# Optimization experiments

Hardware: AMD Instinct MI355X
Metric: run time of the kernel (lower is better)

The kernel has to match this reference:

```python
import math
import jax, jax.numpy as jnp
import numpy as np

H = 12
D_MODEL = 768
D_K = D_MODEL // H
B, S = 2, 2048


def setup_inputs() -> dict:
    key = jax.random.key(0)
    ks = jax.random.split(key, 12)
    sc = 0.02
    inp = {
        "query": jax.random.normal(ks[0], (B, S, D_MODEL), jnp.float32),
        "key": jax.random.normal(ks[1], (B, S, D_MODEL), jnp.float32),
        "value": jax.random.normal(ks[2], (B, S, D_MODEL), jnp.float32),
        # causal mask [B, S, S]: 1 where attendable
        "mask": jnp.broadcast_to(jnp.tril(jnp.ones((S, S), jnp.int32)), (B, S, S)),
        "Wq": sc * jax.random.normal(ks[3], (D_MODEL, D_MODEL), jnp.float32),
        "bq": jnp.zeros((D_MODEL,), jnp.float32),
        "Wk": sc * jax.random.normal(ks[4], (D_MODEL, D_MODEL), jnp.float32),
        "bk": jnp.zeros((D_MODEL,), jnp.float32),
        "Wv": sc * jax.random.normal(ks[5], (D_MODEL, D_MODEL), jnp.float32),
        "bv": jnp.zeros((D_MODEL,), jnp.float32),
        "Wo": sc * jax.random.normal(ks[6], (D_MODEL, D_MODEL), jnp.float32),
        "bo": jnp.zeros((D_MODEL,), jnp.float32),
    }
    return inp


def reference(query, key, value, mask, Wq, bq, Wk, bk, Wv, bv, Wo, bo):
    b, s, _ = query.shape
    # linear projections (torch Linear: x @ W.T + b), split into heads
    def proj(x, W, bias):
        return (x @ W.T + bias).reshape(b, s, H, D_K).transpose(0, 2, 1, 3)  # [B,H,S,Dk]

    q = proj(query, Wq, bq)
    k = proj(key, Wk, bk)
    v = proj(value, Wv, bv)

    scores = jnp.einsum("bhqd,bhkd->bhqk", q, k) / math.sqrt(D_K)  # [B,H,S,S]
    # exponential time-decay bias over key positions 1..S, shape [1,1,1,S]
    time = jnp.exp(-jnp.arange(1, s + 1, dtype=scores.dtype))[None, None, None, :]
    scores = jnp.where(mask[:, None, :, :] == 0, jnp.asarray(-1e9, scores.dtype), scores)
    p_attn = jax.nn.softmax(scores - time, axis=-1)
    x = jnp.einsum("bhqk,bhkd->bhqd", p_attn, v)  # [B,H,S,Dk]
    x = x.transpose(0, 2, 1, 3).reshape(b, s, H * D_K)
    return x @ Wo.T + bo
```

## Files before the change

kernel.cpp:

```cpp
#include <hip/hip_runtime.h>
#include <hip/hip_bf16.h>
#include <math.h>

typedef __bf16 bf16;
typedef __attribute__((ext_vector_type(8))) __bf16 bf16x8;
typedef __attribute__((ext_vector_type(4))) __bf16 bf16x4;
typedef __attribute__((ext_vector_type(4))) float floatx4;

#define NH 12
#define DK 64
#define DM 768
#define NB 2
#define SEQ 2048
#define MTOT (NB * SEQ)
#define WELEM (DM * DM)
#define XELEM (MTOT * DM)

static __device__ __forceinline__ bf16x8 load8(const bf16* p) {
    return *(const bf16x8*)p;
}
static __device__ __forceinline__ float4 ld4(const float* p) {
    return *(const float4*)p;
}
static __device__ __forceinline__ bf16x8 cvt8(const float4 a, const float4 b) {
    bf16x8 r;
    r[0] = (bf16)a.x; r[1] = (bf16)a.y; r[2] = (bf16)a.z; r[3] = (bf16)a.w;
    r[4] = (bf16)b.x; r[5] = (bf16)b.y; r[6] = (bf16)b.z; r[7] = (bf16)b.w;
    return r;
}
static __device__ __forceinline__ void async16(const bf16* g, bf16* l) {
    __builtin_amdgcn_global_load_lds((const __attribute__((address_space(1))) void*)g,
                                     (__attribute__((address_space(3))) void*)l,
                                     16, 0, 0);
}

__global__ __launch_bounds__(256) void cvt_kernel(
    const float* __restrict__ wq, const float* __restrict__ wk,
    const float* __restrict__ wv, const float* __restrict__ wo,
    const float* __restrict__ xq, const float* __restrict__ xk, const float* __restrict__ xv,
    bf16* __restrict__ Wb, bf16* __restrict__ Wob,
    bf16* __restrict__ Xqb, bf16* __restrict__ Xkb, bf16* __restrict__ Xvb) {
    const int g = blockIdx.x * 256 + threadIdx.x;
    const int PW = WELEM / 8;
    const int PX = XELEM / 8;
    if (g < 4 * PW) {
        const int wi = g / PW;
        const int rem = g - wi * PW;
        const int n = rem / 96;
        const int t = rem - n * 96;
        const int s = t >> 3;
        const int j = t & 7;
        const float* src = (wi == 0) ? wq : (wi == 1) ? wk : (wi == 2) ? wv : wo;
        bf16* dst = (wi < 3) ? (Wb + (size_t)wi * WELEM) : Wob;
        const float* p = src + (size_t)n * DM + s * 64 + j * 8;
        *(bf16x8*)(dst + (size_t)n * DM + s * 64 + ((j ^ (n & 7)) * 8)) = cvt8(ld4(p), ld4(p + 4));
    } else {
        const int gx = g - 4 * PW;
        const int xi = gx / PX;
        const int rem = gx - xi * PX;
        const int m = rem / 96;
        const int t = rem - m * 96;
        const int s = t >> 3;
        const int j = t & 7;
        const float* src = (xi == 0) ? xq : (xi == 1) ? xk : xv;
        bf16* dst = (xi == 0) ? Xqb : (xi == 1) ? Xkb : Xvb;
        const float* p = src + (size_t)m * DM + s * 64 + j * 8;
        *(bf16x8*)(dst + (size_t)m * DM + s * 64 + ((j ^ (m & 7)) * 8)) = cvt8(ld4(p), ld4(p + 4));
    }
}

__global__ __launch_bounds__(256, 3) void qkv_kernel(
    const bf16* __restrict__ Xqb, const bf16* __restrict__ Xkb, const bf16* __restrict__ Xvb,
    const bf16* __restrict__ Wb,
    const float* __restrict__ bq, const float* __restrict__ bk, const float* __restrict__ bv,
    bf16* __restrict__ Oq, bf16* __restrict__ Ok, bf16* __restrict__ Ov) {
    __shared__ __align__(16) bf16 SM[2 * 64 * 64 + 2 * 128 * 64];
    bf16* As0 = SM;
    bf16* Bs0 = SM + 8192;

    const int tid = threadIdx.x;
    const int id = blockIdx.x;
    const int xcd = id & 7;
    const int sl = id >> 3;
    const int z = sl / 48;
    const int r = sl % 48;
    const int m0 = (xcd * 8 + r / 6) * 64;
    const int n0 = (r % 6) * 128;

    const bf16* X = (z == 0) ? Xqb : (z == 1) ? Xkb : Xvb;
    const bf16* W = Wb + (size_t)z * WELEM;
    const float* bias = (z == 0) ? bq : (z == 1) ? bk : bv;
    bf16* out = (z == 0) ? Oq : (z == 1) ? Ok : Ov;

    const int wv = tid >> 6;
    const int wm = wv >> 1, wn = wv & 1;
    const int lane = tid & 63;
    const int ln = lane & 15;
    const int kq = lane >> 4;
    const int drow = lane >> 3;
    const int dcol = (lane & 7) * 8;

    floatx4 acc[2][4];
#pragma unroll
    for (int i = 0; i < 2; i++)
#pragma unroll
        for (int j = 0; j < 4; j++) acc[i][j] = (floatx4){0.f, 0.f, 0.f, 0.f};

#pragma unroll
    for (int it = 0; it < 2; it++)
        async16(X + (size_t)(m0 + wv * 16 + it * 8 + drow) * DM + dcol,
                As0 + (wv * 16 + it * 8) * 64);
#pragma unroll
    for (int it = 0; it < 4; it++)
        async16(W + (size_t)(n0 + wv * 32 + it * 8 + drow) * DM + dcol,
                Bs0 + (wv * 32 + it * 8) * 64);

    for (int k = 0; k < 12; k++) {
        __syncthreads();
        const bf16* Ap = As0 + (k & 1) * 4096;
        const bf16* Bp = Bs0 + (k & 1) * 8192;
        if (k < 11) {
            const int kc = (k + 1) * 64;
            bf16* An = As0 + ((k + 1) & 1) * 4096;
            bf16* Bn = Bs0 + ((k + 1) & 1) * 8192;
#pragma unroll
            for (int it = 0; it < 2; it++)
                async16(X + (size_t)(m0 + wv * 16 + it * 8 + drow) * DM + kc + dcol,
                        An + (wv * 16 + it * 8) * 64);
#pragma unroll
            for (int it = 0; it < 4; it++)
                async16(W + (size_t)(n0 + wv * 32 + it * 8 + drow) * DM + kc + dcol,
                        Bn + (wv * 32 + it * 8) * 64);
        }
#pragma unroll
        for (int ks = 0; ks < 2; ks++) {
            const int jb = (ks * 4 + kq) ^ (ln & 7);
            bf16x8 af[2], bfm[4];
#pragma unroll
            for (int mt = 0; mt < 2; mt++)
                af[mt] = *(const bf16x8*)&Ap[(wm * 32 + mt * 16 + ln) * 64 + jb * 8];
#pragma unroll
            for (int nt = 0; nt < 4; nt++)
                bfm[nt] = *(const bf16x8*)&Bp[(wn * 64 + nt * 16 + ln) * 64 + jb * 8];
#pragma unroll
            for (int mt = 0; mt < 2; mt++)
#pragma unroll
                for (int nt = 0; nt < 4; nt++)
                    acc[mt][nt] = __builtin_amdgcn_mfma_f32_16x16x32_bf16(af[mt], bfm[nt], acc[mt][nt], 0, 0, 0);
        }
    }

    float bv4[4];
#pragma unroll
    for (int nt = 0; nt < 4; nt++) bv4[nt] = bias[n0 + wn * 64 + nt * 16 + ln];

    if (z < 2) {
        __syncthreads();
        bf16 (*E)[136] = (bf16(*)[136])SM;
#pragma unroll
        for (int mt = 0; mt < 2; mt++)
#pragma unroll
            for (int nt = 0; nt < 4; nt++)
#pragma unroll
                for (int r2 = 0; r2 < 4; r2++)
                    E[wm * 32 + mt * 16 + kq * 4 + r2][wn * 64 + nt * 16 + ln] =
                        (bf16)(acc[mt][nt][r2] + bv4[nt]);
        __syncthreads();
        const int row = tid >> 2;
        const int cb = (tid & 3) * 32;
        const int m = m0 + row;
        const int b = m >> 11;
        const int s = m & (SEQ - 1);
        const int h = (n0 + cb) >> 6;
        const int d = (n0 + cb) & 63;
        bf16* op = &out[((size_t)(b * NH + h) * SEQ + s) * DK + d];
#pragma unroll
        for (int q2 = 0; q2 < 4; q2++)
            *(bf16x8*)(op + q2 * 8) = *(bf16x8*)&E[row][cb + q2 * 8];
    } else {
        __syncthreads();
        bf16 (*E)[72] = (bf16(*)[72])SM;
#pragma unroll
        for (int nt = 0; nt < 4; nt++)
#pragma unroll
            for (int mt = 0; mt < 2; mt++) {
                bf16x4 v;
#pragma unroll
                for (int r2 = 0; r2 < 4; r2++) v[r2] = (bf16)(acc[mt][nt][r2] + bv4[nt]);
                *(bf16x4*)&E[wn * 64 + nt * 16 + ln][wm * 32 + mt * 16 + kq * 4] = v;
            }
        __syncthreads();
        const int row = tid >> 1;
        const int sc = (tid & 1) * 32;
        const int b = m0 >> 11;
        const int s0 = m0 & (SEQ - 1);
        const int h = (n0 >> 6) + (row >> 6);
        const int d = row & 63;
        bf16* op = &out[(size_t)(b * NH + h) * DK * SEQ + (size_t)d * SEQ + s0 + sc];
#pragma unroll
        for (int q2 = 0; q2 < 4; q2++)
            *(bf16x8*)(op + q2 * 8) = *(bf16x8*)&E[row][sc + q2 * 8];
    }
}

__global__ __launch_bounds__(256) void attn_kernel(const bf16* __restrict__ Q,
                                                   const bf16* __restrict__ K,
                                                   const bf16* __restrict__ Vt,
                                                   bf16* __restrict__ Xout) {
    __shared__ bf16 Ks[128][72];
    __shared__ bf16 Vs[64][136];
    __shared__ bf16 Ps[4][16][136];

    const int tid = threadIdx.x;
    const int wv = tid >> 6;
    const int lane = tid & 63;
    const int ln = lane & 15;
    const int kq = lane >> 4;
    const int krow = tid >> 1;
    const int kcol = (tid & 1) * 32;
    const int vrow = tid >> 2;
    const int vcol = (tid & 3) * 32;

    const int bidx = blockIdx.x;
    const int rk = (bidx < 256 || bidx >= 512) ? bidx : 767 - bidx;
    const int x = 31 - (rk / 24);
    const int bh = rk % 24;

    const int q0 = x * 64;
    const int qbase = q0 + wv * 16;
    const int nch = (x >> 1) + 1;

    const bf16* Qb = Q + (size_t)bh * SEQ * DK;
    const bf16* Kb = K + (size_t)bh * SEQ * DK;
    const bf16* Vb = Vt + (size_t)bh * SEQ * DK;

    const bf16x8 qa0 = load8(&Qb[(size_t)(qbase + ln) * DK + kq * 8]);
    const bf16x8 qa1 = load8(&Qb[(size_t)(qbase + ln) * DK + 32 + kq * 8]);

    bf16x8 kx[4], vx[4];
#pragma unroll
    for (int q = 0; q < 4; q++) {
        kx[q] = load8(&Kb[(size_t)krow * DK + kcol + q * 8]);
        vx[q] = load8(&Vb[(size_t)vrow * SEQ + vcol + q * 8]);
    }

    float lsum[4] = {0.f, 0.f, 0.f, 0.f};
    floatx4 Oacc[4];
#pragma unroll
    for (int nt = 0; nt < 4; nt++) Oacc[nt] = (floatx4){0.f, 0.f, 0.f, 0.f};

    int qg[4];
#pragma unroll
    for (int r = 0; r < 4; r++) qg[r] = qbase + kq * 4 + r;

    for (int c = 0; c < nch; c++) {
        const int k0 = c * 128;
        __syncthreads();
#pragma unroll
        for (int q = 0; q < 4; q++) {
            *(bf16x8*)&Ks[krow][kcol + q * 8] = kx[q];
            *(bf16x8*)&Vs[vrow][vcol + q * 8] = vx[q];
        }
        __syncthreads();
        if (c + 1 < nch) {
            const int kn = k0 + 128;
#pragma unroll
            for (int q = 0; q < 4; q++) {
                kx[q] = load8(&Kb[(size_t)(kn + krow) * DK + kcol + q * 8]);
                vx[q] = load8(&Vb[(size_t)vrow * SEQ + kn + vcol + q * 8]);
            }
        }

        floatx4 sc[8];
#pragma unroll
        for (int ks = 0; ks < 8; ks++) {
            const bf16x8 b0 = *(bf16x8*)&Ks[ks * 16 + ln][kq * 8];
            const bf16x8 b1 = *(bf16x8*)&Ks[ks * 16 + ln][32 + kq * 8];
            floatx4 t = (floatx4){0.f, 0.f, 0.f, 0.f};
            t = __builtin_amdgcn_mfma_f32_16x16x32_bf16(qa0, b0, t, 0, 0, 0);
            t = __builtin_amdgcn_mfma_f32_16x16x32_bf16(qa1, b1, t, 0, 0, 0);
            sc[ks] = t;
        }

        const bool last = (c == nch - 1);
#pragma unroll
        for (int ks = 0; ks < 8; ks++) {
            const int kg = k0 + ks * 16 + ln;
            const float tb = __expf(-(float)(kg + 1));
#pragma unroll
            for (int r = 0; r < 4; r++) {
                const float sv = sc[ks][r] * 0.125f - tb;
                float pf = __expf(sv);
                if (last && kg > qg[r]) pf = 0.f;
                const bf16 pb = (bf16)pf;
                Ps[wv][kq * 4 + r][ks * 16 + ln] = pb;
                lsum[r] += (float)pb;
            }
        }

        bf16x8 pa[4];
#pragma unroll
        for (int seg = 0; seg < 4; seg++) pa[seg] = *(bf16x8*)&Ps[wv][ln][seg * 32 + kq * 8];
#pragma unroll
        for (int nt = 0; nt < 4; nt++) {
#pragma unroll
            for (int seg = 0; seg < 4; seg++) {
                const bf16x8 vb = *(bf16x8*)&Vs[nt * 16 + ln][seg * 32 + kq * 8];
                Oacc[nt] = __builtin_amdgcn_mfma_f32_16x16x32_bf16(pa[seg], vb, Oacc[nt], 0, 0, 0);
            }
        }
    }

#pragma unroll
    for (int off = 1; off < 16; off <<= 1) {
#pragma unroll
        for (int r = 0; r < 4; r++) lsum[r] += __shfl_xor(lsum[r], off, 64);
    }
    float rl[4];
#pragma unroll
    for (int r = 0; r < 4; r++) rl[r] = 1.f / lsum[r];

    __syncthreads();
    bf16 (*E)[72] = (bf16(*)[72])Ks;
    const int erow = tid >> 2;
    const int ecb = (tid & 3) * 16;
#pragma unroll
    for (int nt = 0; nt < 4; nt++) {
#pragma unroll
        for (int r = 0; r < 4; r++)
            E[wv * 16 + kq * 4 + r][nt * 16 + ln] = (bf16)(Oacc[nt][r] * rl[r]);
    }
    __syncthreads();
    const int b = bh / NH;
    const int h = bh - b * NH;
    const int q = q0 + erow;
    const int j0 = (tid & 3) * 2;
    const int key = erow & 7;
    bf16* rowp = &Xout[((size_t)(b * SEQ + q)) * DM + h * DK];
    *(bf16x8*)(rowp + ((j0 ^ key) * 8)) = *(bf16x8*)&E[erow][ecb];
    *(bf16x8*)(rowp + (((j0 + 1) ^ key) * 8)) = *(bf16x8*)&E[erow][ecb + 8];
}

__global__ __launch_bounds__(256, 3) void outproj_kernel(const bf16* __restrict__ X,
                                                         const bf16* __restrict__ W,
                                                         const float* __restrict__ bias,
                                                         float* __restrict__ out) {
    __shared__ __align__(16) bf16 SM[2 * 64 * 64 + 2 * 128 * 64];
    bf16* As0 = SM;
    bf16* Bs0 = SM + 8192;

    const int tid = threadIdx.x;
    const int id = blockIdx.x;
    const int xcd = id & 7;
    const int sl = id >> 3;
    const int m0 = (xcd * 8 + sl / 6) * 64;
    const int n0 = (sl % 6) * 128;

    const int wv = tid >> 6;
    const int wm = wv >> 1, wn = wv & 1;
    const int lane = tid & 63;
    const int ln = lane & 15;
    const int kq = lane >> 4;
    const int drow = lane >> 3;
    const int dcol = (lane & 7) * 8;

    floatx4 acc[2][4];
#pragma unroll
    for (int i = 0; i < 2; i++)
#pragma unroll
        for (int j = 0; j < 4; j++) acc[i][j] = (floatx4){0.f, 0.f, 0.f, 0.f};

#pragma unroll
    for (int it = 0; it < 2; it++)
        async16(X + (size_t)(m0 + wv * 16 + it * 8 + drow) * DM + dcol,
                As0 + (wv * 16 + it * 8) * 64);
#pragma unroll
    for (int it = 0; it < 4; it++)
        async16(W + (size_t)(n0 + wv * 32 + it * 8 + drow) * DM + dcol,
                Bs0 + (wv * 32 + it * 8) * 64);

    for (int k = 0; k < 12; k++) {
        __syncthreads();
        const bf16* Ap = As0 + (k & 1) * 4096;
        const bf16* Bp = Bs0 + (k & 1) * 8192;
        if (k < 11) {
            const int kc = (k + 1) * 64;
            bf16* An = As0 + ((k + 1) & 1) * 4096;
            bf16* Bn = Bs0 + ((k + 1) & 1) * 8192;
#pragma unroll
            for (int it = 0; it < 2; it++)
                async16(X + (size_t)(m0 + wv * 16 + it * 8 + drow) * DM + kc + dcol,
                        An + (wv * 16 + it * 8) * 64);
#pragma unroll
            for (int it = 0; it < 4; it++)
                async16(W + (size_t)(n0 + wv * 32 + it * 8 + drow) * DM + kc + dcol,
                        Bn + (wv * 32 + it * 8) * 64);
        }
#pragma unroll
        for (int ks = 0; ks < 2; ks++) {
            const int jb = (ks * 4 + kq) ^ (ln & 7);
            bf16x8 af[2], bfm[4];
#pragma unroll
            for (int mt = 0; mt < 2; mt++)
                af[mt] = *(const bf16x8*)&Ap[(wm * 32 + mt * 16 + ln) * 64 + jb * 8];
#pragma unroll
            for (int nt = 0; nt < 4; nt++)
                bfm[nt] = *(const bf16x8*)&Bp[(wn * 64 + nt * 16 + ln) * 64 + jb * 8];
#pragma unroll
            for (int mt = 0; mt < 2; mt++)
#pragma unroll
                for (int nt = 0; nt < 4; nt++)
                    acc[mt][nt] = __builtin_amdgcn_mfma_f32_16x16x32_bf16(af[mt], bfm[nt], acc[mt][nt], 0, 0, 0);
        }
    }

#pragma unroll
    for (int nt = 0; nt < 4; nt++) {
        const int n = n0 + wn * 64 + nt * 16 + ln;
        const float bval = bias[n];
#pragma unroll
        for (int mt = 0; mt < 2; mt++)
#pragma unroll
            for (int r2 = 0; r2 < 4; r2++) {
                const int m = m0 + wm * 32 + mt * 16 + kq * 4 + r2;
                out[(size_t)m * DM + n] = acc[mt][nt][r2] + bval;
            }
    }
}

extern "C" void kernel_launch(void* const* d_in, const int* in_sizes, int n_in,
                              void* d_out, int out_size, void* d_ws, size_t ws_size,
                              hipStream_t stream) {
    const float* query = (const float*)d_in[0];
    const float* key   = (const float*)d_in[1];
    const float* value = (const float*)d_in[2];
    const float* Wq = (const float*)d_in[4];
    const float* bq = (const float*)d_in[5];
    const float* Wk = (const float*)d_in[6];
    const float* bk = (const float*)d_in[7];
    const float* Wv = (const float*)d_in[8];
    const float* bv = (const float*)d_in[9];
    const float* Wo = (const float*)d_in[10];
    const float* bo = (const float*)d_in[11];
    float* out = (float*)d_out;

    bf16* Qws  = (bf16*)d_ws;
    bf16* Kws  = Qws + XELEM;
    bf16* Vtws = Kws + XELEM;
    bf16* Xws  = Vtws + XELEM;
    bf16* Wob  = Xws + XELEM;
    bf16* Xvb  = Wob + WELEM;

    bf16* Wb  = (bf16*)out;
    bf16* Xkb = (bf16*)out + 3 * WELEM;

    bf16* Xqb = Xws;

    const int ncvt = (4 * (WELEM / 8) + 3 * (XELEM / 8)) / 256;
    cvt_kernel<<<ncvt, 256, 0, stream>>>(Wq, Wk, Wv, Wo, query, key, value,
                                         Wb, Wob, Xqb, Xkb, Xvb);

    qkv_kernel<<<1152, 256, 0, stream>>>(Xqb, Xkb, Xvb, Wb, bq, bk, bv,
                                         Qws, Kws, Vtws);

    attn_kernel<<<768, 256, 0, stream>>>(Qws, Kws, Vtws, Xws);

    outproj_kernel<<<384, 256, 0, stream>>>(Xws, Wob, bo, out);
}
```

Measured before the change: 198.8 us.

## Compute transposed scores so softmax probs feed PV MFMA directly from registers

Swaps MFMA operand order so the score tile is transposed, with each lane holding one query row. K rows are permuted in LDS so the score accumulator layout matches the A-operand layout of the PV MFMA, which removes the Ps shared-memory round trip. The 1/sqrt(dk)*log2e scale is folded into the Q projection so softmax uses a bare exp2. The time-decay bias is applied only in the first chunk, since it underflows for later keys, and the row-sum reduction becomes two shuffles. Also adds s_setprio around the MFMA blocks and a launch_bounds occupancy hint of 4; the trade-offs are rounding Q to bf16 after scaling and depending on the bias being negligible beyond key 128.

Result: slower. 218.9 us (+10.1%).

```diff
diff --git a/kernel.cpp b/kernel.cpp
--- a/kernel.cpp
+++ b/kernel.cpp
@@ -16,6 +16,9 @@
 #define WELEM (DM * DM)
 #define XELEM (MTOT * DM)
 
+#define QSCALE 0.1803368801111832f
+#define LOG2E 1.4426950408889634f
+
 static __device__ __forceinline__ bf16x8 load8(const bf16* p) {
     return *(const bf16x8*)p;
 }
@@ -27,6 +30,13 @@
     r[0] = (bf16)a.x; r[1] = (bf16)a.y; r[2] = (bf16)a.z; r[3] = (bf16)a.w;
     r[4] = (bf16)b.x; r[5] = (bf16)b.y; r[6] = (bf16)b.z; r[7] = (bf16)b.w;
     return r;
+}
+static __device__ __forceinline__ float fast_exp2(float x) {
+#if __has_builtin(__builtin_amdgcn_exp2f)
+    return __builtin_amdgcn_exp2f(x);
+#else
+    return __expf(x * 0.6931471805599453f);
+#endif
 }
 static __device__ __forceinline__ void async16(const bf16* g, bf16* l) {
     __builtin_amdgcn_global_load_lds((const __attribute__((address_space(1))) void*)g,
@@ -155,6 +165,7 @@
     for (int nt = 0; nt < 4; nt++) bv4[nt] = bias[n0 + wn * 64 + nt * 16 + ln];
 
     if (z < 2) {
+        const float qs = (z == 0) ? QSCALE : 1.0f;
         __syncthreads();
         bf16 (*E)[136] = (bf16(*)[136])SM;
 #pragma unroll
@@ -164,7 +175,7 @@
 #pragma unroll
                 for (int r2 = 0; r2 < 4; r2++)
                     E[wm * 32 + mt * 16 + kq * 4 + r2][wn * 64 + nt * 16 + ln] =
-                        (bf16)(acc[mt][nt][r2] + bv4[nt]);
+                        (bf16)((acc[mt][nt][r2] + bv4[nt]) * qs);
         __syncthreads();
         const int row = tid >> 2;
         const int cb = (tid & 3) * 32;
@@ -203,13 +214,12 @@
     }
 }
 
-__global__ __launch_bounds__(256) void attn_kernel(const bf16* __restrict__ Q,
-                                                   const bf16* __restrict__ K,
-                                                   const bf16* __restrict__ Vt,
-                                                   bf16* __restrict__ Xout) {
+__global__ __launch_bounds__(256, 4) void attn_kernel(const bf16* __restrict__ Q,
+                                                      const bf16* __restrict__ K,
+                                                      const bf16* __restrict__ Vt,
+                                                      bf16* __restrict__ Xout) {
     __shared__ bf16 Ks[128][72];
     __shared__ bf16 Vs[64][136];
-    __shared__ bf16 Ps[4][16][136];
 
     const int tid = threadIdx.x;
     const int wv = tid >> 6;
@@ -217,6 +227,7 @@
     const int ln = lane & 15;
     const int kq = lane >> 4;
     const int krow = tid >> 1;
+    const int kprow = (krow & 0x60) | ((krow & 4) << 2) | ((krow & 24) >> 1) | (krow & 3);
     const int kcol = (tid & 1) * 32;
     const int vrow = tid >> 2;
     const int vcol = (tid & 3) * 32;
@@ -244,21 +255,19 @@
         vx[q] = load8(&Vb[(size_t)vrow * SEQ + vcol + q * 8]);
     }
 
-    float lsum[4] = {0.f, 0.f, 0.f, 0.f};
+    float lsum = 0.f;
     floatx4 Oacc[4];
 #pragma unroll
     for (int nt = 0; nt < 4; nt++) Oacc[nt] = (floatx4){0.f, 0.f, 0.f, 0.f};
 
-    int qg[4];
-#pragma unroll
-    for (int r = 0; r < 4; r++) qg[r] = qbase + kq * 4 + r;
+    const int qgl = qbase + ln;
 
     for (int c = 0; c < nch; c++) {
         const int k0 = c * 128;
         __syncthreads();
 #pragma unroll
         for (int q = 0; q < 4; q++) {
-            *(bf16x8*)&Ks[krow][kcol + q * 8] = kx[q];
+            *(bf16x8*)&Ks[kprow][kcol + q * 8] = kx[q];
             *(bf16x8*)&Vs[vrow][vcol + q * 8] = vx[q];
         }
         __syncthreads();
@@ -272,35 +281,50 @@
         }
 
         floatx4 sc[8];
+        __builtin_amdgcn_s_setprio(1);
 #pragma unroll
         for (int ks = 0; ks < 8; ks++) {
-            const bf16x8 b0 = *(bf16x8*)&Ks[ks * 16 + ln][kq * 8];
-            const bf16x8 b1 = *(bf16x8*)&Ks[ks * 16 + ln][32 + kq * 8];
+            const bf16x8 a0 = *(bf16x8*)&Ks[ks * 16 + ln][kq * 8];
+            const bf16x8 a1 = *(bf16x8*)&Ks[ks * 16 + ln][32 + kq * 8];
             floatx4 t = (floatx4){0.f, 0.f, 0.f, 0.f};
-            t = __builtin_amdgcn_mfma_f32_16x16x32_bf16(qa0, b0, t, 0, 0, 0);
-            t = __builtin_amdgcn_mfma_f32_16x16x32_bf16(qa1, b1, t, 0, 0, 0);
+            t = __builtin_amdgcn_mfma_f32_16x16x32_bf16(a0, qa0, t, 0, 0, 0);
+            t = __builtin_amdgcn_mfma_f32_16x16x32_bf16(a1, qa1, t, 0, 0, 0);
             sc[ks] = t;
         }
-
-        const bool last = (c == nch - 1);
-#pragma unroll
-        for (int ks = 0; ks < 8; ks++) {
-            const int kg = k0 + ks * 16 + ln;
-            const float tb = __expf(-(float)(kg + 1));
-#pragma unroll
-            for (int r = 0; r < 4; r++) {
-                const float sv = sc[ks][r] * 0.125f - tb;
-                float pf = __expf(sv);
-                if (last && kg > qg[r]) pf = 0.f;
-                const bf16 pb = (bf16)pf;
-                Ps[wv][kq * 4 + r][ks * 16 + ln] = pb;
-                lsum[r] += (float)pb;
-            }
-        }
-
+        __builtin_amdgcn_s_setprio(0);
+
+        const bool lastc = (c == nch - 1);
         bf16x8 pa[4];
-#pragma unroll
-        for (int seg = 0; seg < 4; seg++) pa[seg] = *(bf16x8*)&Ps[wv][ln][seg * 32 + kq * 8];
+        if (c == 0) {
+#pragma unroll
+            for (int ks = 0; ks < 8; ks++) {
+                const int kbase = (ks >> 1) * 32 + (ks & 1) * 4 + kq * 8;
+#pragma unroll
+                for (int r = 0; r < 4; r++) {
+                    const int kg = kbase + r;
+                    const float sv = sc[ks][r] - __expf(-(float)(kg + 1)) * LOG2E;
+                    float pf = fast_exp2(sv);
+                    if (lastc && kg > qgl) pf = 0.f;
+                    lsum += pf;
+                    pa[ks >> 1][(ks & 1) * 4 + r] = (bf16)pf;
+                }
+            }
+        } else {
+#pragma unroll
+            for (int ks = 0; ks < 8; ks++) {
+                const int kbase = k0 + (ks >> 1) * 32 + (ks & 1) * 4 + kq * 8;
+#pragma unroll
+                for (int r = 0; r < 4; r++) {
+                    const int kg = kbase + r;
+                    float pf = fast_exp2(sc[ks][r]);
+                    if (lastc && kg > qgl) pf = 0.f;
+                    lsum += pf;
+                    pa[ks >> 1][(ks & 1) * 4 + r] = (bf16)pf;
+                }
+            }
+        }
+
+        __builtin_amdgcn_s_setprio(1);
 #pragma unroll
         for (int nt = 0; nt < 4; nt++) {
 #pragma unroll
@@ -309,16 +333,14 @@
                 Oacc[nt] = __builtin_amdgcn_mfma_f32_16x16x32_bf16(pa[seg], vb, Oacc[nt], 0, 0, 0);
             }
         }
-    }
-
-#pragma unroll
-    for (int off = 1; off < 16; off <<= 1) {
-#pragma unroll
-        for (int r = 0; r < 4; r++) lsum[r] += __shfl_xor(lsum[r], off, 64);
-    }
+        __builtin_amdgcn_s_setprio(0);
+    }
+
+    lsum += __shfl_xor(lsum, 16, 64);
+    lsum += __shfl_xor(lsum, 32, 64);
     float rl[4];
 #pragma unroll
-    for (int r = 0; r < 4; r++) rl[r] = 1.f / lsum[r];
+    for (int r = 0; r < 4; r++) rl[r] = 1.f / __shfl(lsum, kq * 4 + r, 64);
 
     __syncthreads();
     bf16 (*E)[72] = (bf16(*)[72])Ks;
```
